# Kernel tuning notes

Hardware: AMD Instinct MI355X
Metric: run time of the kernel (lower is better)

Reference implementation:

```python
import jax, jax.numpy as jnp
import numpy as np
import math

B, S, H, NH = 2, 4096, 768, 12
HD = H // NH  # 64
LN_EPS = 1e-12


def setup_inputs() -> dict:
    key = jax.random.key(0)
    ks = jax.random.split(key, 6)
    scale = 0.02
    return {
        "hidden_states": jax.random.normal(ks[0], (B, S, H), jnp.float32),
        "attention_mask": jnp.zeros((B, 1, 1, S), jnp.float32),
        "q_w": jax.random.normal(ks[1], (H, H), jnp.float32) * scale,
        "q_b": jnp.zeros((H,), jnp.float32),
        "k_w": jax.random.normal(ks[2], (H, H), jnp.float32) * scale,
        "k_b": jnp.zeros((H,), jnp.float32),
        "v_w": jax.random.normal(ks[3], (H, H), jnp.float32) * scale,
        "v_b": jnp.zeros((H,), jnp.float32),
        "o_w": jax.random.normal(ks[4], (H, H), jnp.float32) * scale,
        "o_b": jnp.zeros((H,), jnp.float32),
        "ln_g": jnp.ones((H,), jnp.float32),
        "ln_b": jnp.zeros((H,), jnp.float32),
    }


def _heads(x):
    # [B,S,H] -> [B,NH,S,HD]
    return x.reshape(B, S, NH, HD).transpose(0, 2, 1, 3)


def reference(hidden_states, attention_mask, q_w, q_b, k_w, k_b, v_w, v_b,
              o_w, o_b, ln_g, ln_b):
    q = _heads(hidden_states @ q_w.T + q_b)
    k = _heads(hidden_states @ k_w.T + k_b)
    v = _heads(hidden_states @ v_w.T + v_b)

    scores = jnp.einsum("bhqd,bhkd->bhqk", q, k) / math.sqrt(HD)
    scores = scores + attention_mask  # additive mask, broadcast [B,1,1,S]
    probs = jax.nn.softmax(scores, axis=-1)  # dropout p=0 in eval
    ctx = jnp.einsum("bhqk,bhkd->bhqd", probs, v)
    ctx = ctx.transpose(0, 2, 1, 3).reshape(B, S, H)

    # Residual block: dense -> (dropout p=0) -> LN(x + input)
    y = ctx @ o_w.T + o_b + hidden_states
    mu = jnp.mean(y, axis=-1, keepdims=True)
    var = jnp.mean(jnp.square(y - mu), axis=-1, keepdims=True)
    out = (y - mu) * jax.lax.rsqrt(var + LN_EPS) * ln_g + ln_b
    return out
```

## Files before the change

kernel.cpp:

```cpp
#include <hip/hip_runtime.h>

typedef __bf16 bf16;
typedef __bf16 bf16x4 __attribute__((ext_vector_type(4)));
typedef __bf16 bf16x8 __attribute__((ext_vector_type(8)));
typedef float f32x4 __attribute__((ext_vector_type(4)));
typedef float f32x16 __attribute__((ext_vector_type(16)));

#define NB 2
#define SEQ 4096
#define HID 768
#define NHEAD 12
#define HDIM 64
#define MTOT (NB * SEQ)
#define LOG2E 1.4426950408889634f

__device__ inline void pack_body(const float* __restrict__ in, bf16* __restrict__ out, int rt) {
    __shared__ alignas(16) bf16 T[16 * 264];
    const int lane = threadIdx.x;
    const int c = lane & 15, g = lane >> 4;
    const float4* in4 = (const float4*)in + (size_t)rt * 16 * (HID / 4);
    for (int chunk = 0; chunk < 3; chunk++) {
#pragma unroll
        for (int i = 0; i < 16; i++) {
            float4 v = in4[(size_t)i * (HID / 4) + chunk * 64 + lane];
            bf16x4 o;
            o[0] = (bf16)v.x; o[1] = (bf16)v.y; o[2] = (bf16)v.z; o[3] = (bf16)v.w;
            *(bf16x4*)&T[i * 264 + lane * 4] = o;
        }
        __syncthreads();
#pragma unroll
        for (int s = 0; s < 8; s++) {
            bf16x8 val = *(const bf16x8*)&T[c * 264 + s * 32 + g * 8];
            *(bf16x8*)(out + (((size_t)rt * 24 + chunk * 8 + s) * 64 + lane) * 8) = val;
        }
        __syncthreads();
    }
}

__global__ __launch_bounds__(64) void pack_a(const float* __restrict__ in, bf16* __restrict__ out) {
    pack_body(in, out, blockIdx.x);
}

__global__ __launch_bounds__(64) void pack_w4(
    const float* __restrict__ w0, const float* __restrict__ w1,
    const float* __restrict__ w2, const float* __restrict__ w3,
    bf16* __restrict__ o0, bf16* __restrict__ o1, bf16* __restrict__ o2, bf16* __restrict__ o3) {
    int y = blockIdx.y;
    const float* in = (y == 0) ? w0 : (y == 1) ? w1 : (y == 2) ? w2 : w3;
    bf16* out = (y == 0) ? o0 : (y == 1) ? o1 : (y == 2) ? o2 : o3;
    pack_body(in, out, blockIdx.x);
}

__global__ __launch_bounds__(256, 2) void qkv_gemm(
    const bf16* __restrict__ Xp,
    const bf16* __restrict__ Wq, const bf16* __restrict__ Wk, const bf16* __restrict__ Wv,
    const float* __restrict__ bq, const float* __restrict__ bk, const float* __restrict__ bv,
    bf16* __restrict__ Qh, bf16* __restrict__ Kh, bf16* __restrict__ Vt)
{
    int z = blockIdx.z;
    const bf16* W = (z == 0) ? Wq : (z == 1) ? Wk : Wv;
    const float* bias = (z == 0) ? bq : (z == 1) ? bk : bv;

    int lane = threadIdx.x & 63;
    int wid  = threadIdx.x >> 6;
    int wm = wid >> 1, wn = wid & 1;
    int g = lane >> 4, c = lane & 15;
    int m0 = blockIdx.y * 128 + wm * 64;
    int n0 = blockIdx.x * 128 + wn * 64;

    f32x4 acc[4][4] = {};
    const bf16* Ap = Xp + ((size_t)(m0 >> 4) * 24) * 512 + (size_t)lane * 8;
    const bf16* Bp = W  + ((size_t)(n0 >> 4) * 24) * 512 + (size_t)lane * 8;

    for (int ks = 0; ks < 24; ks++) {
        bf16x8 a[4], b[4];
#pragma unroll
        for (int i = 0; i < 4; i++) {
            a[i] = *(const bf16x8*)(Ap + ((size_t)i * 24 + ks) * 512);
            b[i] = *(const bf16x8*)(Bp + ((size_t)i * 24 + ks) * 512);
        }
#pragma unroll
        for (int mi = 0; mi < 4; mi++)
#pragma unroll
            for (int ni = 0; ni < 4; ni++)
                acc[mi][ni] = __builtin_amdgcn_mfma_f32_16x16x32_bf16(a[mi], b[ni], acc[mi][ni], 0, 0, 0);
    }

#pragma unroll
    for (int ni = 0; ni < 4; ni++) {
        int n = n0 + ni * 16 + c;
        float bval = bias[n];
        int h = n >> 6, d = n & 63;
#pragma unroll
        for (int mi = 0; mi < 4; mi++) {
#pragma unroll
            for (int j = 0; j < 4; j++) {
                int m = m0 + mi * 16 + g * 4 + j;
                float val = acc[mi][ni][j] + bval;
                int bb = m >> 12, s = m & 4095;
                size_t bhb = (size_t)(bb * NHEAD + h) * SEQ * HDIM;
                if (z == 0) {
                    val *= 0.125f * LOG2E;
                    Qh[bhb + (size_t)s * HDIM + d] = (bf16)val;
                } else if (z == 1) {
                    int fragidx = (((s >> 5) & 1) << 2) | (d >> 4);
                    int lane2 = (s & 31) | (((d >> 3) & 1) << 5);
                    Kh[bhb + (size_t)(s >> 6) * 4096 + fragidx * 512 + lane2 * 8 + (d & 7)] = (bf16)val;
                } else {
                    int fragidx = ((d >> 5) << 2) | ((s >> 4) & 3);
                    int lane2 = (d & 31) | (((s >> 3) & 1) << 5);
                    Vt[bhb + (size_t)(s >> 6) * 4096 + fragidx * 512 + lane2 * 8 + (s & 7)] = (bf16)val;
                }
            }
        }
    }
}

__device__ inline float xhalf_max(float x) {
    float a_ = x, b_ = x;
    asm("v_permlane32_swap_b32 %0, %1" : "+v"(a_), "+v"(b_));
    return fmaxf(a_, b_);
}
__device__ inline float xhalf_sum(float x) {
    float a_ = x, b_ = x;
    asm("v_permlane32_swap_b32 %0, %1" : "+v"(a_), "+v"(b_));
    return a_ + b_;
}

__device__ inline void smax16(f32x16& s, float& m, float& l, f32x16& o0, f32x16& o1) {
    float r[8];
#pragma unroll
    for (int i = 0; i < 8; i++) r[i] = fmaxf(s[i], s[i + 8]);
#pragma unroll
    for (int st = 4; st; st >>= 1)
#pragma unroll
        for (int i = 0; i < st; i++) r[i] = fmaxf(r[i], r[i + st]);
    float t = xhalf_max(r[0]);
    if (__any(t > m + 8.f)) {
        float mn = fmaxf(m, t);
        float al = __builtin_amdgcn_exp2f(m - mn);
        m = mn; l *= al;
#pragma unroll
        for (int i = 0; i < 16; i++) { o0[i] *= al; o1[i] *= al; }
    }
#pragma unroll
    for (int i = 0; i < 16; i++) s[i] = __builtin_amdgcn_exp2f(s[i] - m);
    float q[8];
#pragma unroll
    for (int i = 0; i < 8; i++) q[i] = s[i] + s[i + 8];
#pragma unroll
    for (int st = 4; st; st >>= 1)
#pragma unroll
        for (int i = 0; i < st; i++) q[i] += q[i + st];
    l += xhalf_sum(q[0]);
}

__device__ inline void pconv16(const f32x16& sc, bf16x8* pa) {
    unsigned u[8];
#pragma unroll
    for (int i = 0; i < 8; i++) {
        union { bf16 hh[2]; unsigned uu; } x;
        x.hh[0] = (bf16)sc[i * 2];
        x.hh[1] = (bf16)sc[i * 2 + 1];
        u[i] = x.uu;
    }
    asm("v_permlane32_swap_b32 %0, %1" : "+v"(u[0]), "+v"(u[2]));
    asm("v_permlane32_swap_b32 %0, %1" : "+v"(u[1]), "+v"(u[3]));
    asm("v_permlane32_swap_b32 %0, %1" : "+v"(u[4]), "+v"(u[6]));
    asm("v_permlane32_swap_b32 %0, %1" : "+v"(u[5]), "+v"(u[7]));
    union { unsigned uu[4]; bf16x8 v; } f0, f1;
    f0.uu[0] = u[0]; f0.uu[1] = u[1]; f0.uu[2] = u[2]; f0.uu[3] = u[3];
    f1.uu[0] = u[4]; f1.uu[1] = u[5]; f1.uu[2] = u[6]; f1.uu[3] = u[7];
    pa[0] = f0.v;
    pa[1] = f1.v;
}

__global__ __launch_bounds__(256, 4) void attn_kernel(
    const bf16* __restrict__ Qh, const bf16* __restrict__ Kh, const bf16* __restrict__ Vt,
    const float* __restrict__ mask, bf16* __restrict__ ctxp)
{
    __shared__ float Sm[2][2048];
    __shared__ float Sml[2][128];
    __shared__ alignas(16) bf16 Ep[2][2048];

    const int lane = threadIdx.x & 63;
    const int wid = threadIdx.x >> 6;
    const int qg = wid >> 1;
    const int kp = wid & 1;
    const int lq = lane & 31;
    const int hi = lane >> 5;
    const int bh = blockIdx.x;
    const int b = bh / NHEAD, h = bh % NHEAD;
    const size_t base = (size_t)bh * SEQ * HDIM;
    const int qw = blockIdx.y * 64 + qg * 32;

    bf16x8 qf[4];
#pragma unroll
    for (int dc = 0; dc < 4; dc++)
        qf[dc] = *(const bf16x8*)(Qh + base + (size_t)(qw + lq) * HDIM + dc * 16 + hi * 8);

    const float* maskb = mask + b * SEQ;
    const bf16* kfrag = Kh + base + (size_t)lane * 8;
    const bf16* vfrag = Vt + base + (size_t)lane * 8;

    float m = -3e38f, l = 0.f;
    f32x16 o0 = {}, o1 = {};

    for (int t = 0; t < SEQ / 64; t++) {
        const int kt = 2 * t + kp;
        const size_t tb = (size_t)(kt >> 1) * 4096;
        const int khalf = kt & 1;

        bf16x8 kf[4];
#pragma unroll
        for (int dc = 0; dc < 4; dc++)
            kf[dc] = *(const bf16x8*)(kfrag + tb + (khalf * 4 + dc) * 512);

        f32x16 s = {};
#pragma unroll
        for (int dc = 0; dc < 4; dc++)
            s = __builtin_amdgcn_mfma_f32_32x32x16_bf16(kf[dc], qf[dc], s, 0, 0, 0);

        bf16x8 vf[4];
        vf[0] = *(const bf16x8*)(vfrag + tb + (khalf * 2 + 0) * 512);
        vf[1] = *(const bf16x8*)(vfrag + tb + (khalf * 2 + 1) * 512);
        vf[2] = *(const bf16x8*)(vfrag + tb + (4 + khalf * 2 + 0) * 512);
        vf[3] = *(const bf16x8*)(vfrag + tb + (4 + khalf * 2 + 1) * 512);

        const float* mrow = maskb + kt * 32 + hi * 4;
#pragma unroll
        for (int g = 0; g < 4; g++) {
            f32x4 mk = *(const f32x4*)(mrow + g * 8);
#pragma unroll
            for (int j = 0; j < 4; j++)
                s[g * 4 + j] += mk[j] * LOG2E;
        }

        smax16(s, m, l, o0, o1);
        bf16x8 pa[2];
        pconv16(s, pa);

        o0 = __builtin_amdgcn_mfma_f32_32x32x16_bf16(vf[0], pa[0], o0, 0, 0, 0);
        o0 = __builtin_amdgcn_mfma_f32_32x32x16_bf16(vf[1], pa[1], o0, 0, 0, 0);
        o1 = __builtin_amdgcn_mfma_f32_32x32x16_bf16(vf[2], pa[0], o1, 0, 0, 0);
        o1 = __builtin_amdgcn_mfma_f32_32x32x16_bf16(vf[3], pa[1], o1, 0, 0, 0);
    }

    if (kp == 1) {
#pragma unroll
        for (int i = 0; i < 16; i++) {
            Sm[qg][i * 64 + lane]        = o0[i];
            Sm[qg][(16 + i) * 64 + lane] = o1[i];
        }
        Sml[qg][lane] = m; Sml[qg][64 + lane] = l;
    }
    __syncthreads();
    if (kp == 1) return;

    {
        float mB = Sml[qg][lane], lB = Sml[qg][64 + lane];
        float mm = fmaxf(m, mB);
        float a = __builtin_amdgcn_exp2f(m - mm);
        float bb_ = __builtin_amdgcn_exp2f(mB - mm);
        l = l * a + lB * bb_;
#pragma unroll
        for (int i = 0; i < 16; i++) {
            o0[i] = o0[i] * a + Sm[qg][i * 64 + lane] * bb_;
            o1[i] = o1[i] * a + Sm[qg][(16 + i) * 64 + lane] * bb_;
        }
    }

    float inv = 1.f / l;
    bf16* ep = Ep[qg];
    const int sw = (lq & 7) << 4;
#pragma unroll
    for (int g = 0; g < 4; g++) {
        bf16x4 p0, p1;
#pragma unroll
        for (int j = 0; j < 4; j++) {
            p0[j] = (bf16)(o0[g * 4 + j] * inv);
            p1[j] = (bf16)(o1[g * 4 + j] * inv);
        }
        int colb = g * 16 + hi * 8;
        *(bf16x4*)((char*)ep + lq * 128 + (colb ^ sw)) = p0;
        *(bf16x4*)((char*)ep + lq * 128 + ((64 + colb) ^ sw)) = p1;
    }
    const int c = lane & 15, gg = lane >> 4;
#pragma unroll
    for (int mt = 0; mt < 2; mt++) {
#pragma unroll
        for (int s2 = 0; s2 < 2; s2++) {
            int row = mt * 16 + c;
            int colb = (s2 * 64 + gg * 16) ^ ((row & 7) << 4);
            bf16x8 val = *(const bf16x8*)((const char*)ep + row * 128 + colb);
            size_t mtg = (size_t)((b * SEQ + qw) >> 4) + mt;
            *(bf16x8*)(ctxp + ((mtg * 24 + h * 2 + s2) * 64 + lane) * 8) = val;
        }
    }
}

__global__ __launch_bounds__(256, 2) void oproj_gemm(
    const bf16* __restrict__ Cp, const bf16* __restrict__ Wo, const float* __restrict__ bo,
    const float* __restrict__ hidden, float* __restrict__ y)
{
    int lane = threadIdx.x & 63;
    int wid  = threadIdx.x >> 6;
    int wm = wid >> 1, wn = wid & 1;
    int g = lane >> 4, c = lane & 15;
    int m0 = blockIdx.y * 128 + wm * 64;
    int n0 = blockIdx.x * 128 + wn * 64;

    f32x4 acc[4][4] = {};
    const bf16* Ap = Cp + ((size_t)(m0 >> 4) * 24) * 512 + (size_t)lane * 8;
    const bf16* Bp = Wo + ((size_t)(n0 >> 4) * 24) * 512 + (size_t)lane * 8;

    for (int ks = 0; ks < 24; ks++) {
        bf16x8 a[4], b[4];
#pragma unroll
        for (int i = 0; i < 4; i++) {
            a[i] = *(const bf16x8*)(Ap + ((size_t)i * 24 + ks) * 512);
            b[i] = *(const bf16x8*)(Bp + ((size_t)i * 24 + ks) * 512);
        }
#pragma unroll
        for (int mi = 0; mi < 4; mi++)
#pragma unroll
            for (int ni = 0; ni < 4; ni++)
                acc[mi][ni] = __builtin_amdgcn_mfma_f32_16x16x32_bf16(a[mi], b[ni], acc[mi][ni], 0, 0, 0);
    }

#pragma unroll
    for (int ni = 0; ni < 4; ni++) {
        int n = n0 + ni * 16 + c;
        float bval = bo[n];
#pragma unroll
        for (int mi = 0; mi < 4; mi++) {
#pragma unroll
            for (int j = 0; j < 4; j++) {
                int m = m0 + mi * 16 + g * 4 + j;
                size_t idx = (size_t)m * HID + n;
                y[idx] = acc[mi][ni][j] + bval + hidden[idx];
            }
        }
    }
}

__global__ __launch_bounds__(256) void ln_kernel(
    const float* __restrict__ y, const float* __restrict__ gam,
    const float* __restrict__ bet, float* __restrict__ out)
{
    int row = blockIdx.x * 4 + (threadIdx.x >> 6);
    int lane = threadIdx.x & 63;
    const float* yr = y + (size_t)row * HID;

    float4 v[3];
#pragma unroll
    for (int i = 0; i < 3; i++)
        v[i] = reinterpret_cast<const float4*>(yr)[lane + i * 64];

    float s = 0.f;
#pragma unroll
    for (int i = 0; i < 3; i++) s += v[i].x + v[i].y + v[i].z + v[i].w;
#pragma unroll
    for (int msk = 1; msk < 64; msk <<= 1) s += __shfl_xor(s, msk, 64);
    float mean = s * (1.f / 768.f);

    float q = 0.f;
#pragma unroll
    for (int i = 0; i < 3; i++) {
        float dx = v[i].x - mean, dy = v[i].y - mean, dz = v[i].z - mean, dw = v[i].w - mean;
        q += dx * dx + dy * dy + dz * dz + dw * dw;
    }
#pragma unroll
    for (int msk = 1; msk < 64; msk <<= 1) q += __shfl_xor(q, msk, 64);
    float rstd = rsqrtf(q * (1.f / 768.f) + 1e-12f);

    float* outr = out + (size_t)row * HID;
#pragma unroll
    for (int i = 0; i < 3; i++) {
        float4 gg = reinterpret_cast<const float4*>(gam)[lane + i * 64];
        float4 bb = reinterpret_cast<const float4*>(bet)[lane + i * 64];
        float4 o;
        o.x = (v[i].x - mean) * rstd * gg.x + bb.x;
        o.y = (v[i].y - mean) * rstd * gg.y + bb.y;
        o.z = (v[i].z - mean) * rstd * gg.z + bb.z;
        o.w = (v[i].w - mean) * rstd * gg.w + bb.w;
        reinterpret_cast<float4*>(outr)[lane + i * 64] = o;
    }
}

extern "C" void kernel_launch(void* const* d_in, const int* in_sizes, int n_in,
                              void* d_out, int out_size, void* d_ws, size_t ws_size,
                              hipStream_t stream) {
    const float* hidden = (const float*)d_in[0];
    const float* mask   = (const float*)d_in[1];
    const float* q_w = (const float*)d_in[2];
    const float* q_b = (const float*)d_in[3];
    const float* k_w = (const float*)d_in[4];
    const float* k_b = (const float*)d_in[5];
    const float* v_w = (const float*)d_in[6];
    const float* v_b = (const float*)d_in[7];
    const float* o_w = (const float*)d_in[8];
    const float* o_b = (const float*)d_in[9];
    const float* ln_g = (const float*)d_in[10];
    const float* ln_b = (const float*)d_in[11];
    float* out = (float*)d_out;

    const size_t SZ_X = (size_t)MTOT * HID;
    const size_t SZ_W = (size_t)HID * HID;

    char* ws = (char*)d_ws;
    size_t XB_OFF = 0;
    size_t W_OFF  = XB_OFF + SZ_X * 2;
    size_t QH_OFF = W_OFF + 4 * SZ_W * 2;
    size_t KH_OFF = QH_OFF + SZ_X * 2;
    size_t VT_OFF = KH_OFF + SZ_X * 2;

    bf16* Xp  = (bf16*)(ws + XB_OFF);
    bf16* Wqp = (bf16*)(ws + W_OFF);
    bf16* Wkp = Wqp + SZ_W;
    bf16* Wvp = Wkp + SZ_W;
    bf16* Wop = Wvp + SZ_W;
    bf16* Qh  = (bf16*)(ws + QH_OFF);
    bf16* Kh  = (bf16*)(ws + KH_OFF);
    bf16* Vt  = (bf16*)(ws + VT_OFF);
    bf16* ctxp = (bf16*)(ws + XB_OFF);
    float* y  = (float*)(ws + QH_OFF);

    pack_a<<<dim3(MTOT / 16), 64, 0, stream>>>(hidden, Xp);
    pack_w4<<<dim3(HID / 16, 4), 64, 0, stream>>>(q_w, k_w, v_w, o_w, Wqp, Wkp, Wvp, Wop);

    qkv_gemm<<<dim3(HID / 128, MTOT / 128, 3), 256, 0, stream>>>(
        Xp, Wqp, Wkp, Wvp, q_b, k_b, v_b, Qh, Kh, Vt);

    attn_kernel<<<dim3(NB * NHEAD, SEQ / 64), 256, 0, stream>>>(Qh, Kh, Vt, mask, ctxp);

    oproj_gemm<<<dim3(HID / 128, MTOT / 128), 256, 0, stream>>>(ctxp, Wop, o_b, hidden, y);

    ln_kernel<<<dim3(MTOT / 4), 256, 0, stream>>>(y, ln_g, ln_b, out);
}
```

Measured before the change: 273.4 us.

## Compute softmax row sums via MFMA and pre-permute scaled mask into accumulator

```diff
diff --git a/kernel.cpp b/kernel.cpp
--- a/kernel.cpp
+++ b/kernel.cpp
@@ -49,6 +49,15 @@
     const float* in = (y == 0) ? w0 : (y == 1) ? w1 : (y == 2) ? w2 : w3;
     bf16* out = (y == 0) ? o0 : (y == 1) ? o1 : (y == 2) ? o2 : o3;
     pack_body(in, out, blockIdx.x);
+}
+
+__global__ __launch_bounds__(256) void pack_mask(const float* __restrict__ mask,
+                                                 float* __restrict__ mp) {
+    int idx = blockIdx.x * 256 + threadIdx.x;
+    int b = idx >> 12, r = idx & 4095;
+    int kt = r >> 5, hi = (r >> 4) & 1, i = r & 15;
+    int k = kt * 32 + (i & 3) + 8 * (i >> 2) + 4 * hi;
+    mp[idx] = mask[b * SEQ + k] * LOG2E;
 }
 
 __global__ __launch_bounds__(256, 2) void qkv_gemm(
@@ -121,38 +130,25 @@
     asm("v_permlane32_swap_b32 %0, %1" : "+v"(a_), "+v"(b_));
     return fmaxf(a_, b_);
 }
-__device__ inline float xhalf_sum(float x) {
-    float a_ = x, b_ = x;
-    asm("v_permlane32_swap_b32 %0, %1" : "+v"(a_), "+v"(b_));
-    return a_ + b_;
-}
-
-__device__ inline void smax16(f32x16& s, float& m, float& l, f32x16& o0, f32x16& o1) {
-    float r[8];
-#pragma unroll
-    for (int i = 0; i < 8; i++) r[i] = fmaxf(s[i], s[i + 8]);
-#pragma unroll
-    for (int st = 4; st; st >>= 1)
-#pragma unroll
-        for (int i = 0; i < st; i++) r[i] = fmaxf(r[i], r[i + st]);
-    float t = xhalf_max(r[0]);
+
+__device__ inline void smax16(f32x16& s, float& m, f32x16& o0, f32x16& o1, f32x16& la) {
+    float t0 = fmaxf(fmaxf(s[0], s[1]), s[2]);
+    float t1 = fmaxf(fmaxf(s[3], s[4]), s[5]);
+    float t2 = fmaxf(fmaxf(s[6], s[7]), s[8]);
+    float t3 = fmaxf(fmaxf(s[9], s[10]), s[11]);
+    float t4 = fmaxf(fmaxf(s[12], s[13]), s[14]);
+    float u0 = fmaxf(fmaxf(t0, t1), t2);
+    float u1 = fmaxf(fmaxf(t3, t4), s[15]);
+    float t = xhalf_max(fmaxf(u0, u1));
     if (__any(t > m + 8.f)) {
         float mn = fmaxf(m, t);
         float al = __builtin_amdgcn_exp2f(m - mn);
-        m = mn; l *= al;
-#pragma unroll
-        for (int i = 0; i < 16; i++) { o0[i] *= al; o1[i] *= al; }
+        m = mn;
+#pragma unroll
+        for (int i = 0; i < 16; i++) { o0[i] *= al; o1[i] *= al; la[i] *= al; }
     }
 #pragma unroll
     for (int i = 0; i < 16; i++) s[i] = __builtin_amdgcn_exp2f(s[i] - m);
-    float q[8];
-#pragma unroll
-    for (int i = 0; i < 8; i++) q[i] = s[i] + s[i + 8];
-#pragma unroll
-    for (int st = 4; st; st >>= 1)
-#pragma unroll
-        for (int i = 0; i < st; i++) q[i] += q[i + st];
-    l += xhalf_sum(q[0]);
 }
 
 __device__ inline void pconv16(const f32x16& sc, bf16x8* pa) {
@@ -177,7 +173,7 @@
 
 __global__ __launch_bounds__(256, 4) void attn_kernel(
     const bf16* __restrict__ Qh, const bf16* __restrict__ Kh, const bf16* __restrict__ Vt,
-    const float* __restrict__ mask, bf16* __restrict__ ctxp)
+    const float* __restrict__ maskp, bf16* __restrict__ ctxp)
 {
     __shared__ float Sm[2][2048];
     __shared__ float Sml[2][128];
@@ -199,12 +195,16 @@
     for (int dc = 0; dc < 4; dc++)
         qf[dc] = *(const bf16x8*)(Qh + base + (size_t)(qw + lq) * HDIM + dc * 16 + hi * 8);
 
-    const float* maskb = mask + b * SEQ;
     const bf16* kfrag = Kh + base + (size_t)lane * 8;
     const bf16* vfrag = Vt + base + (size_t)lane * 8;
-
-    float m = -3e38f, l = 0.f;
-    f32x16 o0 = {}, o1 = {};
+    const float* mbase = maskp + ((size_t)b * 128 * 2 + hi) * 16;
+
+    bf16x8 ones;
+#pragma unroll
+    for (int j = 0; j < 8; j++) ones[j] = (bf16)1.0f;
+
+    float m = -3e38f;
+    f32x16 o0 = {}, o1 = {}, la = {};
 
     for (int t = 0; t < SEQ / 64; t++) {
         const int kt = 2 * t + kp;
@@ -216,10 +216,13 @@
         for (int dc = 0; dc < 4; dc++)
             kf[dc] = *(const bf16x8*)(kfrag + tb + (khalf * 4 + dc) * 512);
 
-        f32x16 s = {};
+        f32x16 s = *(const f32x16*)(mbase + (size_t)kt * 32);
+
+        __builtin_amdgcn_s_setprio(1);
 #pragma unroll
         for (int dc = 0; dc < 4; dc++)
             s = __builtin_amdgcn_mfma_f32_32x32x16_bf16(kf[dc], qf[dc], s, 0, 0, 0);
+        __builtin_amdgcn_s_setprio(0);
 
         bf16x8 vf[4];
         vf[0] = *(const bf16x8*)(vfrag + tb + (khalf * 2 + 0) * 512);
@@ -227,24 +230,21 @@
         vf[2] = *(const bf16x8*)(vfrag + tb + (4 + khalf * 2 + 0) * 512);
         vf[3] = *(const bf16x8*)(vfrag + tb + (4 + khalf * 2 + 1) * 512);
 
-        const float* mrow = maskb + kt * 32 + hi * 4;
-#pragma unroll
-        for (int g = 0; g < 4; g++) {
-            f32x4 mk = *(const f32x4*)(mrow + g * 8);
-#pragma unroll
-            for (int j = 0; j < 4; j++)
-                s[g * 4 + j] += mk[j] * LOG2E;
-        }
-
-        smax16(s, m, l, o0, o1);
+        smax16(s, m, o0, o1, la);
         bf16x8 pa[2];
         pconv16(s, pa);
 
+        __builtin_amdgcn_s_setprio(1);
+        la = __builtin_amdgcn_mfma_f32_32x32x16_bf16(ones, pa[0], la, 0, 0, 0);
+        la = __builtin_amdgcn_mfma_f32_32x32x16_bf16(ones, pa[1], la, 0, 0, 0);
         o0 = __builtin_amdgcn_mfma_f32_32x32x16_bf16(vf[0], pa[0], o0, 0, 0, 0);
         o0 = __builtin_amdgcn_mfma_f32_32x32x16_bf16(vf[1], pa[1], o0, 0, 0, 0);
         o1 = __builtin_amdgcn_mfma_f32_32x32x16_bf16(vf[2], pa[0], o1, 0, 0, 0);
         o1 = __builtin_amdgcn_mfma_f32_32x32x16_bf16(vf[3], pa[1], o1, 0, 0, 0);
-    }
+        __builtin_amdgcn_s_setprio(0);
+    }
+
+    float l = la[0];
 
     if (kp == 1) {
 #pragma unroll
@@ -414,6 +414,7 @@
     size_t QH_OFF = W_OFF + 4 * SZ_W * 2;
     size_t KH_OFF = QH_OFF + SZ_X * 2;
     size_t VT_OFF = KH_OFF + SZ_X * 2;
+    size_t MP_OFF = VT_OFF + SZ_X * 2;
 
     bf16* Xp  = (bf16*)(ws + XB_OFF);
     bf16* Wqp = (bf16*)(ws + W_OFF);
@@ -423,16 +424,18 @@
     bf16* Qh  = (bf16*)(ws + QH_OFF);
     bf16* Kh  = (bf16*)(ws + KH_OFF);
     bf16* Vt  = (bf16*)(ws + VT_OFF);
+    float* Mp = (float*)(ws + MP_OFF);
     bf16* ctxp = (bf16*)(ws + XB_OFF);
     float* y  = (float*)(ws + QH_OFF);
 
     pack_a<<<dim3(MTOT / 16), 64, 0, stream>>>(hidden, Xp);
     pack_w4<<<dim3(HID / 16, 4), 64, 0, stream>>>(q_w, k_w, v_w, o_w, Wqp, Wkp, Wvp, Wop);
+    pack_mask<<<dim3(32), 256, 0, stream>>>(mask, Mp);
 
     qkv_gemm<<<dim3(HID / 128, MTOT / 128, 3), 256, 0, stream>>>(
         Xp, Wqp, Wkp, Wvp, q_b, k_b, v_b, Qh, Kh, Vt);
 
-    attn_kernel<<<dim3(NB * NHEAD, SEQ / 64), 256, 0, stream>>>(Qh, Kh, Vt, mask, ctxp);
+    attn_kernel<<<dim3(NB * NHEAD, SEQ / 64), 256, 0, stream>>>(Qh, Kh, Vt, Mp, ctxp);
 
     oproj_gemm<<<dim3(HID / 128, MTOT / 128), 256, 0, stream>>>(ctxp, Wop, o_b, hidden, y);
 
```

After: 290.7 us. 6.3% more time.
